# Performance work log

Measured on AMD Instinct MI355X. Metric: run time of the kernel, lower is better.

## Reference

```python
import jax, jax.numpy as jnp
import numpy as np

B, T_ENC, D_IN = 8, 512, 512
T_DEC, ODIM = 150, 80
D_RNN, PRE, ATTN, LOC, K = 1024, 256, 128, 32, 31
ZONEOUT = 0.1


def setup_inputs() -> dict:
    key = jax.random.key(0)
    ks = jax.random.split(key, 24)
    s = 0.02
    n = jax.random.normal
    inp = {
        "memory": n(ks[0], (B, T_ENC, D_IN), jnp.float32),
        "memory_length": jax.random.randint(ks[1], (B,), 256, T_ENC + 1, jnp.int32),
        "targets": n(ks[2], (B, T_DEC, ODIM), jnp.float32),
        # location-sensitive attention params
        "W_mem": n(ks[3], (ATTN, D_IN), jnp.float32) * s,
        "W_q": n(ks[4], (ATTN, D_RNN), jnp.float32) * s,
        "W_loc": n(ks[5], (ATTN, LOC), jnp.float32) * s,
        "loc_filters": n(ks[6], (LOC, 1, K), jnp.float32) * s,
        "attn_v": n(ks[7], (ATTN,), jnp.float32) * s,
        "attn_b": jnp.zeros((ATTN,), jnp.float32),
        # prenet (80 -> 256 -> 256)
        "pre_W1": n(ks[8], (PRE, ODIM), jnp.float32) * s,
        "pre_b1": jnp.zeros((PRE,), jnp.float32),
        "pre_W2": n(ks[9], (PRE, PRE), jnp.float32) * s,
        "pre_b2": jnp.zeros((PRE,), jnp.float32),
        # LSTM layer 0: input = D_IN + PRE
        "Wi0": n(ks[10], (4 * D_RNN, D_IN + PRE), jnp.float32) * s,
        "Wh0": n(ks[11], (4 * D_RNN, D_RNN), jnp.float32) * s,
        "bl0": jnp.zeros((4 * D_RNN,), jnp.float32),
        # LSTM layer 1
        "Wi1": n(ks[12], (4 * D_RNN, D_RNN), jnp.float32) * s,
        "Wh1": n(ks[13], (4 * D_RNN, D_RNN), jnp.float32) * s,
        "bl1": jnp.zeros((4 * D_RNN,), jnp.float32),
        # projections from zcs = [h_last, att_c] of width D_RNN + D_IN
        "feat_W": n(ks[14], (ODIM, D_RNN + D_IN), jnp.float32) * s,
        "stop_W": n(ks[15], (1, D_RNN + D_IN), jnp.float32) * s,
        "stop_b": jnp.zeros((1,), jnp.float32),
    }
    return inp


def _lstm_cell(x, h, c, Wi, Wh, b):
    g = x @ Wi.T + h @ Wh.T + b
    i, f, gc, o = jnp.split(g, 4, axis=-1)  # torch LSTMCell gate order
    c_new = jax.nn.sigmoid(f) * c + jax.nn.sigmoid(i) * jnp.tanh(gc)
    h_new = jax.nn.sigmoid(o) * jnp.tanh(c_new)
    # zoneout (expected value / eval form)
    return (1.0 - ZONEOUT) * h_new + ZONEOUT * h, (1.0 - ZONEOUT) * c_new + ZONEOUT * c


def reference(memory, memory_length, targets, W_mem, W_q, W_loc, loc_filters,
              attn_v, attn_b, pre_W1, pre_b1, pre_W2, pre_b2,
              Wi0, Wh0, bl0, Wi1, Wh1, bl1, feat_W, stop_W, stop_b):
    b, t_enc, _ = memory.shape
    proc_mem = jnp.einsum('btd,ad->bta', memory, W_mem)           # [B,T,ATTN]
    mask = jnp.arange(t_enc)[None, :] < memory_length[:, None]    # [B,T]

    def step(carry, prev_out):
        h0, c0, h1, c1, att_cum = carry
        # location features: conv over cumulative attention weights
        f = jax.lax.conv_general_dilated(att_cum[:, None, :], loc_filters,
                                         (1,), 'SAME')            # [B,LOC,T]
        loc = jnp.einsum('bct,ac->bta', f, W_loc)                  # [B,T,ATTN]
        q = (h0 @ W_q.T)[:, None, :]                               # [B,1,ATTN]
        e = jnp.einsum('a,bta->bt', attn_v,
                       jnp.tanh(proc_mem + loc + q + attn_b))      # [B,T]
        att_w = jax.nn.softmax(jnp.where(mask, e, -1e9), axis=-1)
        att_c = jnp.einsum('bt,btd->bd', att_w, memory)            # [B,D_IN]
        # prenet on previous output (dropout off: deterministic reference)
        p = jax.nn.relu(prev_out @ pre_W1.T + pre_b1)
        p = jax.nn.relu(p @ pre_W2.T + pre_b2)
        x = jnp.concatenate([att_c, p], axis=1)                    # [B,D_IN+PRE]
        h0, c0 = _lstm_cell(x, h0, c0, Wi0, Wh0, bl0)
        h1, c1 = _lstm_cell(h0, h1, c1, Wi1, Wh1, bl1)
        zcs = jnp.concatenate([h1, att_c], axis=1)                 # use_concate=True
        out = zcs @ feat_W.T                                       # [B,ODIM]
        stop = zcs @ stop_W.T + stop_b                             # [B,1]
        return (h0, c0, h1, c1, att_cum + att_w), (out, stop, att_w)

    z = jnp.zeros((b, D_RNN), memory.dtype)
    init = (z, z, z, z, jnp.zeros((b, t_enc), memory.dtype))
    # teacher forcing: prev_out at step t is targets[t-1], zeros at t=0
    prev_outs = jnp.concatenate(
        [jnp.zeros((b, 1, ODIM), targets.dtype), targets[:, :-1]], axis=1)
    _, (outs, stops, att_ws) = jax.lax.scan(step, init,
                                            jnp.swapaxes(prev_outs, 0, 1))
    before_outs = jnp.swapaxes(outs, 0, 1)         # [B,T_dec,ODIM]
    stops = jnp.swapaxes(stops, 0, 1)[..., 0]      # [B,T_dec]
    att_ws = jnp.swapaxes(att_ws, 0, 1)            # [B,T_dec,T_enc]
    return before_outs, stops, att_ws
```

## Files before the change

kernel.cpp:

```cpp
#include <hip/hip_runtime.h>
#include <hip/hip_fp16.h>
#include <cstdint>
#include <cstddef>


#define NB 256
#define NT 512

#define Bz   8
#define TE   512
#define DINz 512
#define TDz  150
#define ODz  80
#define DRz  1024
#define PREz 256
#define ATz  128
#define LOCz 32
#define KFz  31

#define OF_P    0
#define OF_PM   307200
#define OF_Q    831488
#define OF_U    832512
#define OF_CUM  836608
#define OF_ATTC 840704
#define OF_S    848896
#define OF_INVS 848912
#define OF_H0   848928
#define OF_C0   857120
#define OF_H1   865312
#define OF_C1   873504
#define OF_GH0  881696
#define OF_GH1  914464
#define OF_BAR  947232

#define OFF_X0   0
#define OFF_X1   2048
#define OFF_EX   4096
#define OFF_EXG  4352
#define OFF_CW   4608
#define OFF_QS   4736
#define OFF_PART 4864
#define OFF_UU   5376
#define OFF_F    5632
#define OFF_V    9600
#define OFF_WA   9728
#define OFF_WB   22016
#define OFF_WG1  4608
#define OFF_WG2  20992
#define SM_TOTF  38400

#define AG __HIP_MEMORY_SCOPE_AGENT

__device__ __forceinline__ float ldg_sc1(const float* p){
  return __hip_atomic_load(p, __ATOMIC_RELAXED, AG);
}
__device__ __forceinline__ void stg_sc1(float* p, float v){
  __hip_atomic_store(p, v, __ATOMIC_RELAXED, AG);
}
__device__ __forceinline__ float4 ldg4_sc1(const float* p){
  float4 r; r.x=ldg_sc1(p); r.y=ldg_sc1(p+1); r.z=ldg_sc1(p+2); r.w=ldg_sc1(p+3);
  return r;
}
__device__ __forceinline__ float fsig_(float x){ return 1.f/(1.f + __expf(-x)); }
__device__ __forceinline__ float ftanh_(float x){
  x = fminf(10.f, fmaxf(-10.f, x));
  float e = __expf(2.f*x);
  return (e - 1.f) / (e + 1.f);
}

__device__ __forceinline__ void grid_barrier(int* bar, int target){
  asm volatile("s_waitcnt vmcnt(0) lgkmcnt(0)" ::: "memory");
  __syncthreads();
  const int tid = threadIdx.x;
  if (tid == 0)
    __hip_atomic_store(bar + (blockIdx.x << 4), target, __ATOMIC_RELAXED, AG);
  if (blockIdx.x == 255){
    for (;;){
      int ok = 1;
      if (tid < 256)
        ok = (__hip_atomic_load(bar + (tid << 4), __ATOMIC_RELAXED, AG) >= target);
      if (__syncthreads_and(ok)) break;
    }
    if (tid < 16)
      __hip_atomic_store(bar + 4096 + (tid << 4), target, __ATOMIC_RELAXED, AG);
  }
  if (tid == 0){
    int* ep = bar + 4096 + ((blockIdx.x >> 4) << 4);
    while (__hip_atomic_load(ep, __ATOMIC_RELAXED, AG) < target)
      __builtin_amdgcn_s_sleep(1);
  }
  __syncthreads();
}
__device__ __forceinline__ void grid_barrier_heavy(int* bar, int target){
  asm volatile("s_waitcnt vmcnt(0) lgkmcnt(0)" ::: "memory");
  __syncthreads();
  const int tid = threadIdx.x;
  if (tid == 0)
    __builtin_amdgcn_fence(__ATOMIC_RELEASE, "agent");
  __syncthreads();
  if (tid == 0)
    __hip_atomic_store(bar + (blockIdx.x << 4), target, __ATOMIC_RELAXED, AG);
  if (blockIdx.x == 255){
    for (;;){
      int ok = 1;
      if (tid < 256)
        ok = (__hip_atomic_load(bar + (tid << 4), __ATOMIC_RELAXED, AG) >= target);
      if (__syncthreads_and(ok)) break;
    }
    if (tid < 16)
      __hip_atomic_store(bar + 4096 + (tid << 4), target, __ATOMIC_RELAXED, AG);
  }
  if (tid == 0){
    int* ep = bar + 4096 + ((blockIdx.x >> 4) << 4);
    while (__hip_atomic_load(ep, __ATOMIC_RELAXED, AG) < target)
      __builtin_amdgcn_s_sleep(1);
    __builtin_amdgcn_fence(__ATOMIC_ACQUIRE, "agent");
  }
  __syncthreads();
}

template<int K, bool GM>
__device__ void load_wtile(float* dstf, const float* __restrict__ W, int base){
  __half* dst = (__half*)dstf;
  constexpr int KV = K >> 2;
  constexpr int NV = 32 * KV;
  for (int idx = threadIdx.x; idx < NV; idx += NT){
    int r = idx / KV;
    int c = (idx - r*KV) << 2;
    int grow = GM ? (((r>>3)<<10) + base + (r&7)) : (base + r);
    float4 w = *(const float4*)(W + (size_t)grow*K + c);
    __half* d = dst + (size_t)r*K + c;
    d[0] = __float2half_rn(w.x);
    d[1] = __float2half_rn(w.y);
    d[2] = __float2half_rn(w.z);
    d[3] = __float2half_rn(w.w);
  }
}

__device__ __forceinline__ float reduce_dot(float* sm, float (&acc)[2][8]){
  const int tid = threadIdx.x;
  const int s = tid & 31, pos = tid >> 5;
  #pragma unroll
  for (int i=0;i<2;++i){
    #pragma unroll
    for (int b=0;b<8;++b){
      float v = acc[i][b];
      v += __shfl_xor(v, 16, 64);
      v += __shfl_xor(v,  8, 64);
      v += __shfl_xor(v,  4, 64);
      v += __shfl_xor(v,  2, 64);
      v += __shfl_xor(v,  1, 64);
      acc[i][b] = v;
    }
  }
  if (s == 0){
    #pragma unroll
    for (int i=0;i<2;++i)
      #pragma unroll
      for (int b=0;b<8;++b)
        sm[OFF_EX + ((((pos<<1)+i)<<3) | b)] = acc[i][b];
  }
  __syncthreads();
  return (tid < 256) ? sm[OFF_EX + tid] : 0.f;
}

template<int K, int XMODE>
__device__ float gemm32x8_lds(float* sm, const __half* __restrict__ wlds,
                              const float* __restrict__ xsrc,
                              const float* __restrict__ attc_cur,
                              const float* __restrict__ S_cur,
                              const float* __restrict__ Pt)
{
  constexpr int NCH = K >> 8;
  const int tid = threadIdx.x;
  const int s = tid & 31, pos = tid >> 5;
  float acc[2][8];
  #pragma unroll
  for (int i=0;i<2;++i)
    #pragma unroll
    for (int b=0;b<8;++b) acc[i][b] = 0.f;

  const int xb = tid >> 6, xcol = (tid & 63) << 2;
  float4 xreg[NCH];
  if constexpr (XMODE == 0){
    #pragma unroll
    for (int ch=0; ch<NCH; ++ch)
      xreg[ch] = ldg4_sc1(xsrc + (size_t)xb*K + (ch<<8) + xcol);
  } else {
    float xsc = 1.f / ldg_sc1(S_cur + xb);
    #pragma unroll
    for (int ch=0; ch<2; ++ch){
      float4 v = ldg4_sc1(attc_cur + (xb<<9) + (ch<<8) + xcol);
      v.x*=xsc; v.y*=xsc; v.z*=xsc; v.w*=xsc;
      xreg[ch] = v;
    }
    xreg[2] = *(const float4*)(Pt + (xb<<8) + xcol);
  }
  *(float4*)&sm[OFF_X0 + (xb<<8) + xcol] = xreg[0];
  __syncthreads();
  #pragma unroll
  for (int ch=0; ch<NCH; ++ch){
    if (ch+1 < NCH)
      *(float4*)&sm[(((ch+1)&1) ? OFF_X1 : OFF_X0) + (xb<<8) + xcol] = xreg[(ch+1 < NCH) ? ch+1 : 0];
    const float* xbase = &sm[((ch&1) ? OFF_X1 : OFF_X0)];
    const __half* wch = wlds + (ch<<8);
    #pragma unroll
    for (int j=0;j<2;++j){
      const int k = (j<<7) + (s<<2);
      float4 xv[8];
      #pragma unroll
      for (int b=0;b<8;++b) xv[b] = *(const float4*)&xbase[(b<<8) + k];
      #pragma unroll
      for (int i=0;i<2;++i){
        const int row = (pos<<1) + i;
        uint2 w2 = *(const uint2*)&wch[(size_t)row*K + k];
        __half2 ha = *reinterpret_cast<const __half2*>(&w2.x);
        __half2 hb = *reinterpret_cast<const __half2*>(&w2.y);
        float2 fa = __half22float2(ha);
        float2 fb = __half22float2(hb);
        #pragma unroll
        for (int b=0;b<8;++b){
          acc[i][b] = fmaf(fa.x, xv[b].x, acc[i][b]);
          acc[i][b] = fmaf(fa.y, xv[b].y, acc[i][b]);
          acc[i][b] = fmaf(fb.x, xv[b].z, acc[i][b]);
          acc[i][b] = fmaf(fb.y, xv[b].w, acc[i][b]);
        }
      }
    }
    __syncthreads();
  }
  return reduce_dot(sm, acc);
}

__device__ __forceinline__ float prefetch_gh(const float* gh, int u0){
  const int tid = threadIdx.x;
  if (tid >= 256) return 0.f;
  int row32 = tid >> 3, b = tid & 7;
  int gate = row32 >> 3, ul = row32 & 7;
  return ldg_sc1(&gh[(((gate<<10) + u0 + ul)<<3) + b]);
}
__device__ __forceinline__ float prefetch_h(const float* h, int u0){
  const int tid = threadIdx.x;
  if (tid >= 64) return 0.f;
  return ldg_sc1(&h[((tid&7)<<10) + u0 + (tid>>3)]);
}

__device__ void lstm_epilogue(float* sm, float dot, float ghb,
                              const float* __restrict__ bias, float hold,
                              float* __restrict__ h, float* __restrict__ c, int u0)
{
  const int tid = threadIdx.x;
  if (tid < 256){
    int row32 = tid >> 3;
    int gate = row32 >> 3, ul = row32 & 7;
    sm[OFF_EXG + tid] = dot + bias[(gate<<10) + u0 + ul] + ghb;
  }
  __syncthreads();
  if (tid < 64){
    float gi = sm[OFF_EXG + tid];
    float gf = sm[OFF_EXG + 64 + tid];
    float gg = sm[OFF_EXG + 128 + tid];
    float go = sm[OFF_EXG + 192 + tid];
    int ul2 = tid >> 3, b2 = tid & 7;
    int hi = (b2<<10) + u0 + ul2;
    float co = c[hi];
    float cn = fsig_(gf)*co + fsig_(gi)*ftanh_(gg);
    float hn = fsig_(go)*ftanh_(cn);
    c[hi] = 0.9f*cn + 0.1f*co;
    stg_sc1(&h[hi], 0.9f*hn + 0.1f*hold);
  }
}

__device__ void outstop_wave(int rr, int tp, int par,
    const float* __restrict__ feat_W, const float* __restrict__ stop_W,
    const float* __restrict__ stop_b, const float* __restrict__ h1,
    const float* __restrict__ attc, const float* __restrict__ iSw,
    float* __restrict__ d_out)
{
  if (rr >= 648) return;
  int b = rr / 81, r = rr - 81*b;
  int lane = threadIdx.x & 63;
  const float4* Wr = (const float4*)((r < 80) ? (feat_W + (size_t)r*1536) : stop_W);
  float inv = ldg_sc1(iSw + (par<<3) + b);
  float acc = 0.f, acc2 = 0.f;
  #pragma unroll
  for (int j=0;j<4;++j){
    int p = lane + (j<<6);
    float4 w = Wr[p], x = ldg4_sc1(h1 + (b<<10) + (p<<2));
    acc = fmaf(w.x,x.x, fmaf(w.y,x.y, fmaf(w.z,x.z, fmaf(w.w,x.w, acc))));
  }
  #pragma unroll
  for (int j=4;j<6;++j){
    int p = lane + (j<<6);
    float4 w = Wr[p], x = ldg4_sc1(attc + (par<<12) + (b<<9) + ((p-256)<<2));
    acc2 = fmaf(w.x,x.x, fmaf(w.y,x.y, fmaf(w.z,x.z, fmaf(w.w,x.w, acc2))));
  }
  acc += acc2 * inv;
  acc += __shfl_down(acc, 32, 64);
  acc += __shfl_down(acc, 16, 64);
  acc += __shfl_down(acc,  8, 64);
  acc += __shfl_down(acc,  4, 64);
  acc += __shfl_down(acc,  2, 64);
  acc += __shfl_down(acc,  1, 64);
  if (lane == 0){
    if (r < 80) d_out[((size_t)b*TDz + tp)*ODz + r] = acc;
    else        d_out[96000 + (size_t)b*TDz + tp] = acc + stop_b[0];
  }
}

extern "C" __global__ void __launch_bounds__(NT, 1) dec_kernel(
  const float* __restrict__ memory, const int* __restrict__ mlen, const float* __restrict__ targets,
  const float* __restrict__ W_mem, const float* __restrict__ W_q, const float* __restrict__ W_loc,
  const float* __restrict__ loc_f, const float* __restrict__ attn_v, const float* __restrict__ attn_b,
  const float* __restrict__ pre_W1, const float* __restrict__ pre_b1,
  const float* __restrict__ pre_W2, const float* __restrict__ pre_b2,
  const float* __restrict__ Wi0, const float* __restrict__ Wh0, const float* __restrict__ bl0,
  const float* __restrict__ Wi1, const float* __restrict__ Wh1, const float* __restrict__ bl1,
  const float* __restrict__ feat_W, const float* __restrict__ stop_W, const float* __restrict__ stop_b,
  float* __restrict__ d_out, float* __restrict__ ws)
{
  __shared__ float sm[SM_TOTF];
  const int blk = blockIdx.x, tid = threadIdx.x;

  float* Pw   = ws + OF_P;
  float* pmT  = ws + OF_PM;
  float* qw   = ws + OF_Q;
  float* uw   = ws + OF_U;
  float* cum  = ws + OF_CUM;
  float* attc = ws + OF_ATTC;
  float* Sw   = ws + OF_S;
  float* iSw  = ws + OF_INVS;
  float* h0 = ws + OF_H0; float* c0 = ws + OF_C0;
  float* h1 = ws + OF_H1; float* c1 = ws + OF_C1;
  float* gh0 = ws + OF_GH0; float* gh1 = ws + OF_GH1;
  int* bar = (int*)(ws + OF_BAR);
  int bt = 0;

  const bool is_attn = (blk < 128);
  const int ab  = blk >> 4;
  const int ai0 = (blk & 15) << 5;
  const int il  = tid & 31;
  const int ag  = tid >> 5;

  {
    const int gs = NB*NT;
    const int gid = blk*NT + tid;
    for (int i = gid; i < 98304; i += gs) h0[i] = 0.f;
    for (int i = gid; i < 1024;  i += gs) qw[i]  = 0.f;
    for (int i = gid; i < 4096;  i += gs) cum[i] = 0.f;
    for (int i = gid; i < 8192;  i += gs) attc[i] = 0.f;
    if (gid < 32) Sw[gid] = 0.f;

    if (blk < 124){
      load_wtile<768, true >(&sm[OFF_WA], Wi0, blk<<3);
      load_wtile<1024,false>(&sm[OFF_WB], Wh0, blk<<5);
    } else if (blk < 128){
      load_wtile<768, true >(&sm[OFF_WA], Wi0, blk<<3);
      load_wtile<1024,false>(&sm[OFF_WB], W_q, (blk-124)<<5);
    } else {
      load_wtile<1024,false>(&sm[OFF_WG1], Wh1, (blk-128)<<5);
      load_wtile<1024,true >(&sm[OFF_WG2], Wi1, (blk-128)<<3);
    }

    if (is_attn){
      float pacc[8];
      #pragma unroll
      for (int j=0;j<8;++j) pacc[j] = 0.f;
      for (int dc=0; dc<4; ++dc){
        for (int idx = tid; idx < 4096; idx += NT){
          int r = idx >> 7, d = idx & 127;
          sm[r*129 + d] = memory[(size_t)((ab<<9)+ai0+r)*DINz + (dc<<7) + d];
        }
        __syncthreads();
        #pragma unroll
        for (int j=0;j<8;++j){
          int a = (ag<<3) + j;
          const float* wr = W_mem + (size_t)a*DINz + (dc<<7);
          const float* mr = &sm[il*129];
          float acc = 0.f;
          for (int d=0; d<128; d+=4){
            acc = fmaf(mr[d  ], wr[d  ], acc);
            acc = fmaf(mr[d+1], wr[d+1], acc);
            acc = fmaf(mr[d+2], wr[d+2], acc);
            acc = fmaf(mr[d+3], wr[d+3], acc);
          }
          pacc[j] += acc;
        }
        __syncthreads();
      }
      #pragma unroll
      for (int j=0;j<8;++j){
        int a = (ag<<3) + j;
        pmT[((size_t)blk<<12) + (a<<5) + il] = pacc[j] + attn_b[a];
      }
      for (int idx = tid; idx < ATz*KFz; idx += NT){
        int a = idx / KFz, k = idx - a*KFz;
        float s2 = 0.f;
        #pragma unroll
        for (int c2=0;c2<LOCz;++c2) s2 = fmaf(W_loc[(a<<5)+c2], loc_f[c2*KFz+k], s2);
        sm[OFF_F + idx] = s2;
      }
      if (tid < 128) sm[OFF_V + tid] = attn_v[tid];
      __syncthreads();
    }

    const int th = tid >> 8, t2 = tid & 255, base = th << 9;
    for (int it=0; it<3; ++it){
      int pp = (blk<<1) + th + (it<<9);
      bool act = pp < 1200;
      if (act && t2 < ODz){
        int tt = pp >> 3, bb = pp & 7;
        sm[base + t2] = (tt==0) ? 0.f : targets[((size_t)bb*TDz + (tt-1))*ODz + t2];
      }
      __syncthreads();
      if (act){
        float a1 = pre_b1[t2];
        for (int k=0;k<ODz;++k) a1 = fmaf(pre_W1[t2*ODz+k], sm[base+k], a1);
        sm[base + 128 + t2] = fmaxf(a1, 0.f);
      }
      __syncthreads();
      if (act){
        float a2 = pre_b2[t2];
        for (int k=0;k<PREz;++k) a2 = fmaf(pre_W2[(t2<<8)+k], sm[base+128+k], a2);
        Pw[((size_t)pp<<8) + t2] = fmaxf(a2, 0.f);
      }
      __syncthreads();
    }
  }
  grid_barrier_heavy(bar, ++bt);

  for (int t = 0; t < TDz; ++t){
    const int cur = t & 1, prv = cur ^ 1;

    if (is_attn){
      if (tid < 62){
        int gi = ai0 - 15 + tid;
        sm[OFF_CW + tid] = (gi >= 0 && gi < TE) ? ldg_sc1(&cum[(ab<<9)+gi]) : 0.f;
      }
      if (tid < 128) sm[OFF_QS + tid] = ldg_sc1(&qw[(tid<<3) + ab]);
      __syncthreads();
      float part = 0.f;
      #pragma unroll
      for (int j=0;j<8;++j){
        int a = (ag<<3) + j;
        const float* fb = &sm[OFF_F + a*KFz];
        float conv = 0.f;
        #pragma unroll
        for (int k=0;k<KFz;++k) conv = fmaf(fb[k], sm[OFF_CW + il + k], conv);
        float pv = pmT[((size_t)blk<<12) + (a<<5) + il];
        part = fmaf(sm[OFF_V + a], ftanh_(pv + sm[OFF_QS + a] + conv), part);
      }
      sm[OFF_PART + (il<<4) + ag] = part;
      __syncthreads();
      if (tid < 32){
        float e = 0.f;
        #pragma unroll
        for (int k=0;k<16;++k) e += sm[OFF_PART + (tid<<4) + k];
        int gi = ai0 + tid;
        float uu = (gi < mlen[ab]) ? __expf(e) : 0.f;
        stg_sc1(&uw[(ab<<9)+gi], uu);
        sm[OFF_UU + tid] = uu;
      }
      __syncthreads();
      if (tid == 0){
        float ssum = 0.f;
        #pragma unroll
        for (int k=0;k<32;++k) ssum += sm[OFF_UU + k];
        atomicAdd(&Sw[(cur<<3)+ab], ssum);
      }
      {
        float acc = 0.f;
        const float* mrow = memory + (size_t)((ab<<9)+ai0)*DINz + tid;
        #pragma unroll 8
        for (int i=0;i<32;++i)
          acc = fmaf(sm[OFF_UU + i], mrow[(size_t)i*DINz], acc);
        atomicAdd(&attc[(cur<<12) + (ab<<9) + tid], acc);
      }
    } else {
      const int tile = blk - 128;
      float dot = gemm32x8_lds<1024,0>(sm, (const __half*)&sm[OFF_WG1], h1,
                                       nullptr, nullptr, nullptr);
      if (tid < 256) stg_sc1(&gh1[(tile<<8) + tid], dot);
    }
    grid_barrier(bar, ++bt);

    if (blk < 128){
      const int u0 = blk << 3;
      float ghb  = prefetch_gh(gh0, u0);
      float hold = prefetch_h(h0, u0);
      float dot = gemm32x8_lds<768,1>(sm, (const __half*)&sm[OFF_WA], nullptr,
                                      attc + (cur<<12), Sw + (cur<<3),
                                      Pw + ((size_t)t<<11));
      lstm_epilogue(sm, dot, ghb, bl0, hold, h0, c0, u0);
    } else if (blk < 136){
      const int b = blk - 128;
      float Sv = __hip_atomic_load(&Sw[(cur<<3)+b], __ATOMIC_RELAXED, AG);
      float inv = 1.f / Sv;
      if (tid == 0) stg_sc1(&iSw[(cur<<3)+b], inv);
      for (int i = tid; i < TE; i += NT){
        float u = ldg_sc1(&uw[(b<<9)+i]);
        float w = u * inv;
        d_out[97200 + ((size_t)b*TDz + t)*TE + i] = w;
        stg_sc1(&cum[(b<<9)+i], ldg_sc1(&cum[(b<<9)+i]) + w);
      }
    } else if (blk < 217){
      if (t > 0)
        outstop_wave((blk-136)*8 + (tid>>6), t-1, prv,
                     feat_W, stop_W, stop_b, h1, attc, iSw, d_out);
    }
    grid_barrier(bar, ++bt);

    if (blk < 124){
      float dot = gemm32x8_lds<1024,0>(sm, (const __half*)&sm[OFF_WB], h0,
                                       nullptr, nullptr, nullptr);
      if (tid < 256) stg_sc1(&gh0[(blk<<8) + tid], dot);
    } else if (blk < 128){
      const int rt = blk - 124;
      float dot = gemm32x8_lds<1024,0>(sm, (const __half*)&sm[OFF_WB], h0,
                                       nullptr, nullptr, nullptr);
      if (tid < 256) stg_sc1(&qw[(rt<<8) + tid], dot);
      const int zbase = (prv<<12) + (rt<<10);
      for (int i = tid; i < 1024; i += NT) stg_sc1(&attc[zbase + i], 0.f);
      if (rt == 0 && tid < 8) stg_sc1(&Sw[(prv<<3)+tid], 0.f);
    } else {
      const int u0 = (blk - 128) << 3;
      const int blkL = blk - 128;
      {
        const int xb = tid >> 6, xcol = (tid & 63) << 2;
        const float* wr = Wh0 + (size_t)(3968 + blkL)*1024;
        float tp_ = 0.f;
        #pragma unroll
        for (int c=0;c<4;++c){
          float4 w = *(const float4*)(wr + (c<<8) + xcol);
          float4 x = ldg4_sc1(h0 + (xb<<10) + (c<<8) + xcol);
          tp_ = fmaf(w.x,x.x, fmaf(w.y,x.y, fmaf(w.z,x.z, fmaf(w.w,x.w, tp_))));
        }
        tp_ += __shfl_down(tp_, 32, 64);
        tp_ += __shfl_down(tp_, 16, 64);
        tp_ += __shfl_down(tp_,  8, 64);
        tp_ += __shfl_down(tp_,  4, 64);
        tp_ += __shfl_down(tp_,  2, 64);
        tp_ += __shfl_down(tp_,  1, 64);
        if ((tid & 63) == 0) stg_sc1(&gh0[((3968 + blkL)<<3) + xb], tp_);
      }
      float ghb  = prefetch_gh(gh1, u0);
      float hold = prefetch_h(h1, u0);
      float dot = gemm32x8_lds<1024,0>(sm, (const __half*)&sm[OFF_WG2], h0,
                                       nullptr, nullptr, nullptr);
      lstm_epilogue(sm, dot, ghb, bl1, hold, h1, c1, u0);
    }
    grid_barrier(bar, ++bt);
  }

  if (blk >= 136 && blk < 217)
    outstop_wave((blk-136)*8 + (tid>>6), TDz-1, 1,
                 feat_W, stop_W, stop_b, h1, attc, iSw, d_out);
}

extern "C" void kernel_launch(void* const* d_in, const int* in_sizes, int n_in,
                              void* d_out, int out_size, void* d_ws, size_t ws_size,
                              hipStream_t stream)
{
  (void)in_sizes; (void)n_in; (void)out_size; (void)ws_size;
  (void)hipMemsetAsync((char*)d_ws + (size_t)OF_BAR*4, 0, 18432, stream);
  dec_kernel<<<dim3(NB), dim3(NT), 0, stream>>>(
    (const float*)d_in[0],  (const int*)d_in[1],   (const float*)d_in[2],
    (const float*)d_in[3],  (const float*)d_in[4],  (const float*)d_in[5],
    (const float*)d_in[6],  (const float*)d_in[7],  (const float*)d_in[8],
    (const float*)d_in[9],  (const float*)d_in[10], (const float*)d_in[11], (const float*)d_in[12],
    (const float*)d_in[13], (const float*)d_in[14], (const float*)d_in[15],
    (const float*)d_in[16], (const float*)d_in[17], (const float*)d_in[18],
    (const float*)d_in[19], (const float*)d_in[20], (const float*)d_in[21],
    (float*)d_out, (float*)d_ws);
}
```

Measured before the change: 4.777 ms.

## Prefetch LSTM0 operands before barrier and let idle blocks skip barrier wait

Attention blocks now prefetch the LSTM layer-0 inputs (gh0 bias partials, old h0, prenet row) before the mid-step grid barrier, so that latency overlaps the attention work. Blocks that do not need the attention results (136..254, except the master) only signal arrival instead of waiting at that barrier. The partial-sum LDS array is padded to stride 17 to avoid bank conflicts, with OFF_UU shifted to make room. The extra h0 loads are unused for K=768 and add register pressure. The relaxed barrier depends on the later phases of those blocks not reading data from the current phase.

```diff
diff --git a/kernel.cpp b/kernel.cpp
--- a/kernel.cpp
+++ b/kernel.cpp
@@ -41,7 +41,7 @@
 #define OFF_CW   4608
 #define OFF_QS   4736
 #define OFF_PART 4864
-#define OFF_UU   5376
+#define OFF_UU   5408
 #define OFF_F    5632
 #define OFF_V    9600
 #define OFF_WA   9728
@@ -91,6 +91,12 @@
       __builtin_amdgcn_s_sleep(1);
   }
   __syncthreads();
+}
+__device__ __forceinline__ void grid_barrier_arrive(int* bar, int target){
+  asm volatile("s_waitcnt vmcnt(0) lgkmcnt(0)" ::: "memory");
+  __syncthreads();
+  if (threadIdx.x == 0)
+    __hip_atomic_store(bar + (blockIdx.x << 4), target, __ATOMIC_RELAXED, AG);
 }
 __device__ __forceinline__ void grid_barrier_heavy(int* bar, int target){
   asm volatile("s_waitcnt vmcnt(0) lgkmcnt(0)" ::: "memory");
@@ -170,7 +176,7 @@
                               const float* __restrict__ xsrc,
                               const float* __restrict__ attc_cur,
                               const float* __restrict__ S_cur,
-                              const float* __restrict__ Pt)
+                              const float4* __restrict__ xpre)
 {
   constexpr int NCH = K >> 8;
   const int tid = threadIdx.x;
@@ -195,7 +201,8 @@
       v.x*=xsc; v.y*=xsc; v.z*=xsc; v.w*=xsc;
       xreg[ch] = v;
     }
-    xreg[2] = *(const float4*)(Pt + (xb<<8) + xcol);
+    #pragma unroll
+    for (int ch=2; ch<NCH; ++ch) xreg[ch] = xpre[ch-2];
   }
   *(float4*)&sm[OFF_X0 + (xb<<8) + xcol] = xreg[0];
   __syncthreads();
@@ -433,7 +440,19 @@
   for (int t = 0; t < TDz; ++t){
     const int cur = t & 1, prv = cur ^ 1;
 
+    float p2_ghb = 0.f, p2_hold = 0.f;
+    float4 p2_x[5];
     if (is_attn){
+      {
+        const int u0 = blk << 3;
+        const int xb = tid >> 6, xcol = (tid & 63) << 2;
+        p2_ghb  = prefetch_gh(gh0, u0);
+        p2_hold = prefetch_h(h0, u0);
+        p2_x[0] = *(const float4*)(Pw + ((size_t)t<<11) + (xb<<8) + xcol);
+        #pragma unroll
+        for (int c=0;c<4;++c)
+          p2_x[1+c] = ldg4_sc1(h0 + (xb<<10) + (c<<8) + xcol);
+      }
       if (tid < 62){
         int gi = ai0 - 15 + tid;
         sm[OFF_CW + tid] = (gi >= 0 && gi < TE) ? ldg_sc1(&cum[(ab<<9)+gi]) : 0.f;
@@ -451,12 +470,12 @@
         float pv = pmT[((size_t)blk<<12) + (a<<5) + il];
         part = fmaf(sm[OFF_V + a], ftanh_(pv + sm[OFF_QS + a] + conv), part);
       }
-      sm[OFF_PART + (il<<4) + ag] = part;
+      sm[OFF_PART + il*17 + ag] = part;
       __syncthreads();
       if (tid < 32){
         float e = 0.f;
         #pragma unroll
-        for (int k=0;k<16;++k) e += sm[OFF_PART + (tid<<4) + k];
+        for (int k=0;k<16;++k) e += sm[OFF_PART + tid*17 + k];
         int gi = ai0 + tid;
         float uu = (gi < mlen[ab]) ? __expf(e) : 0.f;
         stg_sc1(&uw[(ab<<9)+gi], uu);
@@ -483,16 +502,14 @@
                                        nullptr, nullptr, nullptr);
       if (tid < 256) stg_sc1(&gh1[(tile<<8) + tid], dot);
     }
-    grid_barrier(bar, ++bt);
+    if (blk < 136 || blk == 255) grid_barrier(bar, ++bt);
+    else                         grid_barrier_arrive(bar, ++bt);
 
     if (blk < 128){
       const int u0 = blk << 3;
-      float ghb  = prefetch_gh(gh0, u0);
-      float hold = prefetch_h(h0, u0);
       float dot = gemm32x8_lds<768,1>(sm, (const __half*)&sm[OFF_WA], nullptr,
-                                      attc + (cur<<12), Sw + (cur<<3),
-                                      Pw + ((size_t)t<<11));
-      lstm_epilogue(sm, dot, ghb, bl0, hold, h0, c0, u0);
+                                      attc + (cur<<12), Sw + (cur<<3), p2_x);
+      lstm_epilogue(sm, dot, p2_ghb, bl0, p2_hold, h0, c0, u0);
     } else if (blk < 136){
       const int b = blk - 128;
       float Sv = __hip_atomic_load(&Sw[(cur<<3)+b], __ATOMIC_RELAXED, AG);
```

Measured after the change: 4.767 ms. About the same (-0.2%).
